# Optimization experiments

Hardware: AMD Instinct MI355X
Metric: run time of the kernel (lower is better)

Reference implementation:

```python
import jax, jax.numpy as jnp
import numpy as np

B, S, D, H, E, K = 2, 1024, 512, 2048, 64, 2
EPS = 1e-5


def setup_inputs() -> dict:
    key = jax.random.key(0)
    ks = jax.random.split(key, 5)
    s = 0.02  # small init scale for stability
    return {
        "x": jax.random.normal(ks[0], (B, S, D), dtype=jnp.float32),
        "Wg": jax.random.normal(ks[1], (D, E), dtype=jnp.float32) * s,
        "bg": jnp.zeros((E,), dtype=jnp.float32),
        "W1": jax.random.normal(ks[2], (E, D, H), dtype=jnp.float32) * s,
        "b1": jnp.zeros((E, H), dtype=jnp.float32),
        "W2": jax.random.normal(ks[3], (E, H, D), dtype=jnp.float32) * s,
        "b2": jnp.zeros((E, D), dtype=jnp.float32),
        "gamma": jnp.ones((D,), dtype=jnp.float32),
        "beta": jnp.zeros((D,), dtype=jnp.float32),
    }


def reference(x, Wg, bg, W1, b1, W2, b2, gamma, beta):
    # Gating: softmax over experts, keep top-k weights, zero the rest (scatter)
    probs = jax.nn.softmax(x @ Wg + bg, axis=-1)          # [B,S,E]
    topk_vals, topk_idx = jax.lax.top_k(probs, K)          # [B,S,K]
    sparse_w = jnp.sum(
        jax.nn.one_hot(topk_idx, E, dtype=probs.dtype) * topk_vals[..., None],
        axis=-2,
    )                                                      # [B,S,E]

    # Dense MoE: run every expert FFN on every token (faithful to source)
    h = jax.nn.relu(jnp.einsum('bsd,edh->bseh', x, W1) + b1)   # [B,S,E,H]
    expert_out = jnp.einsum('bseh,ehd->bsed', h, W2) + b2      # [B,S,E,D]

    # Weighted combine + residual
    out = jnp.einsum('bse,bsed->bsd', sparse_w, expert_out) + x

    # LayerNorm (eps=1e-5, elementwise affine)
    mu = out.mean(-1, keepdims=True)
    var = ((out - mu) ** 2).mean(-1, keepdims=True)
    return (out - mu) * jax.lax.rsqrt(var + EPS) * gamma + beta
```

## Files before the change

kernel.cpp:

```cpp
#include <hip/hip_runtime.h>
#include <hip/hip_bf16.h>

#define NTOK 2048
#define DIM 512
#define HID 2048
#define NEXP 64
#define NSLICE 8
#define HSLICE 256
#define TT 64
#define LN_EPS 1e-5f

#define WS_OFF 0
#define HS_OFF 20480
#define SMEM_BYTES 53248

typedef __bf16 bf16x8 __attribute__((ext_vector_type(8)));
typedef float f32x4 __attribute__((ext_vector_type(4)));

__global__ void init_kernel(float4* __restrict__ accb, int* __restrict__ counts) {
    int i = blockIdx.x * blockDim.x + threadIdx.x;
    accb[i] = make_float4(0.f, 0.f, 0.f, 0.f);
    if (i < NEXP) counts[i] = 0;
}

__global__ void gate_kernel(const float* __restrict__ x,
                            const float* __restrict__ Wg,
                            const float* __restrict__ bg,
                            int* __restrict__ counts,
                            int* __restrict__ btok,
                            float* __restrict__ bw) {
    const int t = blockIdx.x;
    const int lane = threadIdx.x;
    __shared__ float xs[DIM];
    const float4* xrow = (const float4*)(x + (size_t)t * DIM);
    ((float4*)xs)[lane] = xrow[lane];
    ((float4*)xs)[lane + 64] = xrow[lane + 64];
    __syncthreads();

    float acc = bg[lane];
    #pragma unroll 8
    for (int d = 0; d < DIM; d++) acc += xs[d] * Wg[d * NEXP + lane];

    float m = acc;
    #pragma unroll
    for (int off = 32; off; off >>= 1) m = fmaxf(m, __shfl_xor(m, off));
    float p = __expf(acc - m);
    float ssum = p;
    #pragma unroll
    for (int off = 32; off; off >>= 1) ssum += __shfl_xor(ssum, off);
    float prob = p / ssum;

    float v1 = prob; int i1 = lane;
    #pragma unroll
    for (int off = 32; off; off >>= 1) {
        float ov = __shfl_xor(v1, off);
        int   oi = __shfl_xor(i1, off);
        if (ov > v1 || (ov == v1 && oi < i1)) { v1 = ov; i1 = oi; }
    }
    float v2 = (lane == i1) ? -1e30f : prob; int i2 = lane;
    #pragma unroll
    for (int off = 32; off; off >>= 1) {
        float ov = __shfl_xor(v2, off);
        int   oi = __shfl_xor(i2, off);
        if (ov > v2 || (ov == v2 && oi < i2)) { v2 = ov; i2 = oi; }
    }

    if (lane == 0) {
        int s0 = atomicAdd(&counts[i1], 1);
        btok[i1 * NTOK + s0] = t;  bw[i1 * NTOK + s0] = v1;
        int s1 = atomicAdd(&counts[i2], 1);
        btok[i2 * NTOK + s1] = t;  bw[i2 * NTOK + s1] = v2;
    }
}

__device__ __forceinline__ void stage_w(const float* __restrict__ src, size_t rs,
                                        __bf16* __restrict__ wsb, int tid) {
    #pragma unroll
    for (int kh = 0; kh < 2; kh++) {
        float v[16];
        #pragma unroll
        for (int u = 0; u < 16; u++)
            v[u] = src[(size_t)(kh * 16 + u) * rs + tid];
        #pragma unroll
        for (int kg = 0; kg < 2; kg++) {
            bf16x8 pk;
            #pragma unroll
            for (int j = 0; j < 8; j++) pk[j] = (__bf16)v[kg * 8 + j];
            *(bf16x8*)(wsb + tid * 40 + (kh * 2 + kg) * 8) = pk;
        }
    }
}

__global__ __launch_bounds__(256, 3) void ffn_kernel(
    const float* __restrict__ x,
    const float* __restrict__ W1, const float* __restrict__ b1,
    const float* __restrict__ W2, const float* __restrict__ b2,
    const int* __restrict__ counts,
    const int* __restrict__ btok, const float* __restrict__ bw,
    float* __restrict__ accb)
{
    __shared__ char smem[SMEM_BYTES];
    __bf16* wsb = (__bf16*)(smem + WS_OFF);

    const int e = blockIdx.x >> 3;
    const int s = blockIdx.x & 7;
    const int n = counts[e];
    if (n <= 0) return;

    const int tid  = threadIdx.x;
    const int lane = tid & 63;
    const int wid  = tid >> 6;
    const int lq   = lane >> 4;
    const int lm   = lane & 15;

    const float* W1e = W1 + (size_t)e * DIM * HID;
    const float* W2e = W2 + (size_t)e * HID * DIM;
    const int*   btoke = btok + e * NTOK;
    const float* bwe   = bw   + e * NTOK;

    for (int t0 = 0; t0 < n; t0 += TT) {
        const int tiln = min(TT, n - t0);

        int  toks[4];
        bool tv[4];
        #pragma unroll
        for (int mt = 0; mt < 4; mt++) {
            int tr = mt * 16 + lm;
            tv[mt] = tr < tiln;
            toks[mt] = tv[mt] ? btoke[t0 + tr] : 0;
        }

        f32x4 acc[4][4];
        #pragma unroll
        for (int i = 0; i < 4; i++)
            #pragma unroll
            for (int j = 0; j < 4; j++) acc[i][j] = (f32x4)0.0f;

        for (int ks = 0; ks < 16; ks++) {
            __syncthreads();
            stage_w(W1e + (size_t)(ks * 32) * HID + s * HSLICE, HID, wsb, tid);
            __syncthreads();

            bf16x8 af[4];
            #pragma unroll
            for (int mt = 0; mt < 4; mt++) {
                if (tv[mt]) {
                    const float* xp = x + (size_t)toks[mt] * DIM + ks * 32 + lq * 8;
                    float4 f0 = *(const float4*)(xp);
                    float4 f1 = *(const float4*)(xp + 4);
                    bf16x8 v;
                    v[0]=(__bf16)f0.x; v[1]=(__bf16)f0.y; v[2]=(__bf16)f0.z; v[3]=(__bf16)f0.w;
                    v[4]=(__bf16)f1.x; v[5]=(__bf16)f1.y; v[6]=(__bf16)f1.z; v[7]=(__bf16)f1.w;
                    af[mt] = v;
                } else {
                    af[mt] = (bf16x8)0.0f;
                }
            }
            #pragma unroll
            for (int nt = 0; nt < 4; nt++) {
                bf16x8 bfv = *(const bf16x8*)(wsb + (wid * 64 + nt * 16 + lm) * 40 + lq * 8);
                #pragma unroll
                for (int mt = 0; mt < 4; mt++)
                    acc[nt][mt] = __builtin_amdgcn_mfma_f32_16x16x32_bf16(
                        af[mt], bfv, acc[nt][mt], 0, 0, 0);
            }
        }

        __syncthreads();
        #pragma unroll
        for (int nt = 0; nt < 4; nt++) {
            int hloc0 = wid * 64 + nt * 16 + lm;
            float b1v = b1[e * HID + s * HSLICE + hloc0];
            #pragma unroll
            for (int mt = 0; mt < 4; mt++) {
                #pragma unroll
                for (int r = 0; r < 4; r++) {
                    int tr = mt * 16 + lq * 4 + r;
                    float v = fmaxf(acc[nt][mt][r] + b1v, 0.f);
                    *(__bf16*)(smem + HS_OFF + tr * 512 +
                               (((hloc0 >> 3) ^ (tr & 7)) * 16) + (hloc0 & 7) * 2) = (__bf16)v;
                }
            }
        }

        for (int dh = 0; dh < 2; dh++) {
            f32x4 yacc[4][4];
            #pragma unroll
            for (int i = 0; i < 4; i++)
                #pragma unroll
                for (int j = 0; j < 4; j++) yacc[i][j] = (f32x4)0.0f;

            for (int ks = 0; ks < 8; ks++) {
                __syncthreads();
                stage_w(W2e + (size_t)(s * HSLICE + ks * 32) * DIM + dh * 256, DIM, wsb, tid);
                __syncthreads();

                bf16x8 af[4];
                int kcA = ks * 4 + lq;
                #pragma unroll
                for (int mt = 0; mt < 4; mt++) {
                    int tr = mt * 16 + lm;
                    af[mt] = *(const bf16x8*)(smem + HS_OFF + tr * 512 + ((kcA ^ (tr & 7)) * 16));
                }
                #pragma unroll
                for (int nt = 0; nt < 4; nt++) {
                    bf16x8 bfv = *(const bf16x8*)(wsb + (wid * 64 + nt * 16 + lm) * 40 + lq * 8);
                    #pragma unroll
                    for (int mt = 0; mt < 4; mt++)
                        yacc[nt][mt] = __builtin_amdgcn_mfma_f32_16x16x32_bf16(
                            af[mt], bfv, yacc[nt][mt], 0, 0, 0);
                }
            }
            float b2s[4];
            #pragma unroll
            for (int nt = 0; nt < 4; nt++) {
                int d = dh * 256 + wid * 64 + nt * 16 + lm;
                b2s[nt] = (s == 0) ? b2[e * DIM + d] : 0.f;
            }
            #pragma unroll
            for (int mt = 0; mt < 4; mt++) {
                #pragma unroll
                for (int r = 0; r < 4; r++) {
                    int tr = mt * 16 + lq * 4 + r;
                    if (tr < tiln) {
                        int tok = btoke[t0 + tr];
                        float w = bwe[t0 + tr];
                        float* dst = accb + (size_t)tok * DIM;
                        #pragma unroll
                        for (int nt = 0; nt < 4; nt++) {
                            int d = dh * 256 + wid * 64 + nt * 16 + lm;
                            atomicAdd(dst + d, w * (yacc[nt][mt][r] + b2s[nt]));
                        }
                    }
                }
            }
        }
        __syncthreads();
    }
}

__global__ void ln_kernel(const float* __restrict__ x,
                          const float* __restrict__ accb,
                          const float* __restrict__ gamma,
                          const float* __restrict__ beta,
                          float* __restrict__ out) {
    const int t = blockIdx.x;
    const int tid = threadIdx.x;
    __shared__ float red[8];
    const size_t base = (size_t)t * DIM;
    float v0 = x[base + tid] + accb[base + tid];
    float v1 = x[base + 256 + tid] + accb[base + 256 + tid];
    float s  = v0 + v1;
    float sq = v0 * v0 + v1 * v1;
    #pragma unroll
    for (int off = 32; off; off >>= 1) { s += __shfl_xor(s, off); sq += __shfl_xor(sq, off); }
    if ((tid & 63) == 0) { red[tid >> 6] = s; red[4 + (tid >> 6)] = sq; }
    __syncthreads();
    float S  = red[0] + red[1] + red[2] + red[3];
    float SQ = red[4] + red[5] + red[6] + red[7];
    float mu  = S * (1.f / DIM);
    float var = SQ * (1.f / DIM) - mu * mu;
    float inv = rsqrtf(var + LN_EPS);
    out[base + tid]       = (v0 - mu) * inv * gamma[tid]       + beta[tid];
    out[base + 256 + tid] = (v1 - mu) * inv * gamma[256 + tid] + beta[256 + tid];
}

extern "C" void kernel_launch(void* const* d_in, const int* in_sizes, int n_in,
                              void* d_out, int out_size, void* d_ws, size_t ws_size,
                              hipStream_t stream) {
    const float* x     = (const float*)d_in[0];
    const float* Wg    = (const float*)d_in[1];
    const float* bg    = (const float*)d_in[2];
    const float* W1    = (const float*)d_in[3];
    const float* b1    = (const float*)d_in[4];
    const float* W2    = (const float*)d_in[5];
    const float* b2    = (const float*)d_in[6];
    const float* gamma = (const float*)d_in[7];
    const float* beta  = (const float*)d_in[8];

    char* ws = (char*)d_ws;
    int*   counts = (int*)ws;
    int*   btok   = (int*)(ws + 4096);
    float* bwv    = (float*)(ws + 4096 + 524288);
    float* accb   = (float*)(ws + 4096 + 2 * 524288);

    init_kernel<<<1024, 256, 0, stream>>>((float4*)accb, counts);
    gate_kernel<<<NTOK, 64, 0, stream>>>(x, Wg, bg, counts, btok, bwv);
    ffn_kernel<<<NEXP * NSLICE, 256, 0, stream>>>(x, W1, b1, W2, b2,
                                                  counts, btok, bwv, accb);
    ln_kernel<<<NTOK, 256, 0, stream>>>(x, accb, gamma, beta, (float*)d_out);
}
```

Baseline: 745.7 us.

## Double-buffer weight staging with register prefetch and single-barrier MFMA loops

Weight tiles for both FFN GEMMs move to two LDS buffers. The next tile is loaded into registers as float4 and written to the idle buffer while MFMAs run on the current one, so each step needs one lgkmcnt barrier instead of two syncthreads. Activation loads from x are also prefetched one k-step ahead, and the W2 loop is flattened into 16 steps so the pipeline spans both D halves. The weight LDS layout gets an XOR swizzle with coalesced float4 global reads. The cost is more LDS and registers, with launch bounds lowered from 3 to 2 blocks per CU, which reduces occupancy.

```diff
diff --git a/kernel.cpp b/kernel.cpp
--- a/kernel.cpp
+++ b/kernel.cpp
@@ -10,12 +10,19 @@
 #define TT 64
 #define LN_EPS 1e-5f
 
-#define WS_OFF 0
-#define HS_OFF 20480
-#define SMEM_BYTES 53248
+#define WS0_OFF 0
+#define WS1_OFF 20480
+#define HS_OFF  40960
+#define SMEM_BYTES 73728
 
 typedef __bf16 bf16x8 __attribute__((ext_vector_type(8)));
 typedef float f32x4 __attribute__((ext_vector_type(4)));
+
+#define LGKM_BARRIER() do { \
+    asm volatile("s_waitcnt lgkmcnt(0)" ::: "memory"); \
+    __builtin_amdgcn_s_barrier(); \
+    asm volatile("" ::: "memory"); \
+} while (0)
 
 __global__ void init_kernel(float4* __restrict__ accb, int* __restrict__ counts) {
     int i = blockIdx.x * blockDim.x + threadIdx.x;
@@ -73,25 +80,55 @@
     }
 }
 
-__device__ __forceinline__ void stage_w(const float* __restrict__ src, size_t rs,
-                                        __bf16* __restrict__ wsb, int tid) {
-    #pragma unroll
-    for (int kh = 0; kh < 2; kh++) {
-        float v[16];
-        #pragma unroll
-        for (int u = 0; u < 16; u++)
-            v[u] = src[(size_t)(kh * 16 + u) * rs + tid];
-        #pragma unroll
-        for (int kg = 0; kg < 2; kg++) {
-            bf16x8 pk;
-            #pragma unroll
-            for (int j = 0; j < 8; j++) pk[j] = (__bf16)v[kg * 8 + j];
-            *(bf16x8*)(wsb + tid * 40 + (kh * 2 + kg) * 8) = pk;
-        }
-    }
-}
-
-__global__ __launch_bounds__(256, 3) void ffn_kernel(
+__device__ __forceinline__ int ws_off(int col, int kg) {
+    return col * 40 + ((kg ^ ((col >> 3) & 3)) << 3);
+}
+
+__device__ __forceinline__ void wload(const float* __restrict__ src, size_t rs,
+                                      int wid, int lane, float4 v[8]) {
+    const float* p = src + (size_t)(wid * 8) * rs + lane * 4;
+    #pragma unroll
+    for (int u = 0; u < 8; u++) v[u] = *(const float4*)(p + (size_t)u * rs);
+}
+
+__device__ __forceinline__ void wstore(__bf16* __restrict__ wsb,
+                                       int wid, int lane, const float4 v[8]) {
+    #pragma unroll
+    for (int j = 0; j < 4; j++) {
+        bf16x8 pk;
+        #pragma unroll
+        for (int u = 0; u < 8; u++) {
+            const float* f = (const float*)&v[u];
+            pk[u] = (__bf16)f[j];
+        }
+        *(bf16x8*)(wsb + ws_off(lane * 4 + j, wid)) = pk;
+    }
+}
+
+__device__ __forceinline__ void aload(const float* __restrict__ x,
+                                      const int toks[4], int ks, int lq,
+                                      float4 ar[4][2]) {
+    #pragma unroll
+    for (int mt = 0; mt < 4; mt++) {
+        const float* xp = x + (size_t)toks[mt] * DIM + ks * 32 + lq * 8;
+        ar[mt][0] = *(const float4*)xp;
+        ar[mt][1] = *(const float4*)(xp + 4);
+    }
+}
+
+__device__ __forceinline__ void acvt(const float4 ar[4][2], bf16x8 af[4]) {
+    #pragma unroll
+    for (int mt = 0; mt < 4; mt++) {
+        bf16x8 v;
+        const float* f0 = (const float*)&ar[mt][0];
+        const float* f1 = (const float*)&ar[mt][1];
+        #pragma unroll
+        for (int j = 0; j < 4; j++) { v[j] = (__bf16)f0[j]; v[4 + j] = (__bf16)f1[j]; }
+        af[mt] = v;
+    }
+}
+
+__global__ __launch_bounds__(256, 2) void ffn_kernel(
     const float* __restrict__ x,
     const float* __restrict__ W1, const float* __restrict__ b1,
     const float* __restrict__ W2, const float* __restrict__ b2,
@@ -100,7 +137,8 @@
     float* __restrict__ accb)
 {
     __shared__ char smem[SMEM_BYTES];
-    __bf16* wsb = (__bf16*)(smem + WS_OFF);
+    __bf16* ws0 = (__bf16*)(smem + WS0_OFF);
+    __bf16* ws1 = (__bf16*)(smem + WS1_OFF);
 
     const int e = blockIdx.x >> 3;
     const int s = blockIdx.x & 7;
@@ -113,21 +151,19 @@
     const int lq   = lane >> 4;
     const int lm   = lane & 15;
 
-    const float* W1e = W1 + (size_t)e * DIM * HID;
-    const float* W2e = W2 + (size_t)e * HID * DIM;
+    const float* W1s = W1 + (size_t)e * DIM * HID + s * HSLICE;
+    const float* W2s = W2 + ((size_t)e * HID + (size_t)s * HSLICE) * DIM;
     const int*   btoke = btok + e * NTOK;
     const float* bwe   = bw   + e * NTOK;
 
     for (int t0 = 0; t0 < n; t0 += TT) {
         const int tiln = min(TT, n - t0);
 
-        int  toks[4];
-        bool tv[4];
+        int toks[4];
         #pragma unroll
         for (int mt = 0; mt < 4; mt++) {
             int tr = mt * 16 + lm;
-            tv[mt] = tr < tiln;
-            toks[mt] = tv[mt] ? btoke[t0 + tr] : 0;
+            toks[mt] = (tr < tiln) ? btoke[t0 + tr] : btoke[t0];
         }
 
         f32x4 acc[4][4];
@@ -136,37 +172,40 @@
             #pragma unroll
             for (int j = 0; j < 4; j++) acc[i][j] = (f32x4)0.0f;
 
+        float4 wv[8];
+        float4 ar[4][2];
+
+        wload(W1s, HID, wid, lane, wv);
+        aload(x, toks, 0, lq, ar);
+        wstore(ws0, wid, lane, wv);
+        wload(W1s + (size_t)32 * HID, HID, wid, lane, wv);
+        LGKM_BARRIER();
+        int cur = 0;
+
         for (int ks = 0; ks < 16; ks++) {
-            __syncthreads();
-            stage_w(W1e + (size_t)(ks * 32) * HID + s * HSLICE, HID, wsb, tid);
-            __syncthreads();
-
             bf16x8 af[4];
-            #pragma unroll
-            for (int mt = 0; mt < 4; mt++) {
-                if (tv[mt]) {
-                    const float* xp = x + (size_t)toks[mt] * DIM + ks * 32 + lq * 8;
-                    float4 f0 = *(const float4*)(xp);
-                    float4 f1 = *(const float4*)(xp + 4);
-                    bf16x8 v;
-                    v[0]=(__bf16)f0.x; v[1]=(__bf16)f0.y; v[2]=(__bf16)f0.z; v[3]=(__bf16)f0.w;
-                    v[4]=(__bf16)f1.x; v[5]=(__bf16)f1.y; v[6]=(__bf16)f1.z; v[7]=(__bf16)f1.w;
-                    af[mt] = v;
-                } else {
-                    af[mt] = (bf16x8)0.0f;
-                }
-            }
+            acvt(ar, af);
+            if (ks < 15) aload(x, toks, ks + 1, lq, ar);
+
+            const __bf16* wr = cur ? ws1 : ws0;
             #pragma unroll
             for (int nt = 0; nt < 4; nt++) {
-                bf16x8 bfv = *(const bf16x8*)(wsb + (wid * 64 + nt * 16 + lm) * 40 + lq * 8);
+                bf16x8 bfv = *(const bf16x8*)(wr + ws_off(wid * 64 + nt * 16 + lm, lq));
                 #pragma unroll
                 for (int mt = 0; mt < 4; mt++)
                     acc[nt][mt] = __builtin_amdgcn_mfma_f32_16x16x32_bf16(
                         af[mt], bfv, acc[nt][mt], 0, 0, 0);
             }
-        }
-
-        __syncthreads();
+            if (ks < 15) {
+                __bf16* ww = cur ? ws0 : ws1;
+                wstore(ww, wid, lane, wv);
+                if (ks < 14)
+                    wload(W1s + (size_t)((ks + 2) * 32) * HID, HID, wid, lane, wv);
+                LGKM_BARRIER();
+                cur ^= 1;
+            }
+        }
+
         #pragma unroll
         for (int nt = 0; nt < 4; nt++) {
             int hloc0 = wid * 64 + nt * 16 + lm;
@@ -183,59 +222,75 @@
             }
         }
 
-        for (int dh = 0; dh < 2; dh++) {
-            f32x4 yacc[4][4];
-            #pragma unroll
-            for (int i = 0; i < 4; i++)
-                #pragma unroll
-                for (int j = 0; j < 4; j++) yacc[i][j] = (f32x4)0.0f;
-
-            for (int ks = 0; ks < 8; ks++) {
-                __syncthreads();
-                stage_w(W2e + (size_t)(s * HSLICE + ks * 32) * DIM + dh * 256, DIM, wsb, tid);
-                __syncthreads();
-
-                bf16x8 af[4];
-                int kcA = ks * 4 + lq;
+        f32x4 yacc[4][4];
+        wload(W2s, DIM, wid, lane, wv);
+        wstore(ws0, wid, lane, wv);
+        wload(W2s + (size_t)32 * DIM, DIM, wid, lane, wv);
+        LGKM_BARRIER();
+        cur = 0;
+
+        for (int u = 0; u < 16; u++) {
+            const int kk = u & 7, dh = u >> 3;
+            if (kk == 0) {
+                #pragma unroll
+                for (int i = 0; i < 4; i++)
+                    #pragma unroll
+                    for (int j = 0; j < 4; j++) yacc[i][j] = (f32x4)0.0f;
+            }
+
+            bf16x8 af[4];
+            const int kcA = kk * 4 + lq;
+            #pragma unroll
+            for (int mt = 0; mt < 4; mt++) {
+                int tr = mt * 16 + lm;
+                af[mt] = *(const bf16x8*)(smem + HS_OFF + tr * 512 + ((kcA ^ (tr & 7)) * 16));
+            }
+            const __bf16* wr = cur ? ws1 : ws0;
+            #pragma unroll
+            for (int nt = 0; nt < 4; nt++) {
+                bf16x8 bfv = *(const bf16x8*)(wr + ws_off(wid * 64 + nt * 16 + lm, lq));
+                #pragma unroll
+                for (int mt = 0; mt < 4; mt++)
+                    yacc[nt][mt] = __builtin_amdgcn_mfma_f32_16x16x32_bf16(
+                        af[mt], bfv, yacc[nt][mt], 0, 0, 0);
+            }
+            if (u < 15) {
+                __bf16* ww = cur ? ws0 : ws1;
+                wstore(ww, wid, lane, wv);
+                if (u < 14) {
+                    const int un = u + 2;
+                    wload(W2s + (size_t)((un & 7) * 32) * DIM + (un >> 3) * 256,
+                          DIM, wid, lane, wv);
+                }
+                LGKM_BARRIER();
+                cur ^= 1;
+            }
+            if (kk == 7) {
+                float b2s[4];
+                #pragma unroll
+                for (int nt = 0; nt < 4; nt++) {
+                    int d = dh * 256 + wid * 64 + nt * 16 + lm;
+                    b2s[nt] = (s == 0) ? b2[e * DIM + d] : 0.f;
+                }
                 #pragma unroll
                 for (int mt = 0; mt < 4; mt++) {
-                    int tr = mt * 16 + lm;
-                    af[mt] = *(const bf16x8*)(smem + HS_OFF + tr * 512 + ((kcA ^ (tr & 7)) * 16));
-                }
-                #pragma unroll
-                for (int nt = 0; nt < 4; nt++) {
-                    bf16x8 bfv = *(const bf16x8*)(wsb + (wid * 64 + nt * 16 + lm) * 40 + lq * 8);
                     #pragma unroll
-                    for (int mt = 0; mt < 4; mt++)
-                        yacc[nt][mt] = __builtin_amdgcn_mfma_f32_16x16x32_bf16(
-                            af[mt], bfv, yacc[nt][mt], 0, 0, 0);
-                }
-            }
-            float b2s[4];
-            #pragma unroll
-            for (int nt = 0; nt < 4; nt++) {
-                int d = dh * 256 + wid * 64 + nt * 16 + lm;
-                b2s[nt] = (s == 0) ? b2[e * DIM + d] : 0.f;
-            }
-            #pragma unroll
-            for (int mt = 0; mt < 4; mt++) {
-                #pragma unroll
-                for (int r = 0; r < 4; r++) {
-                    int tr = mt * 16 + lq * 4 + r;
-                    if (tr < tiln) {
-                        int tok = btoke[t0 + tr];
-                        float w = bwe[t0 + tr];
-                        float* dst = accb + (size_t)tok * DIM;
-                        #pragma unroll
-                        for (int nt = 0; nt < 4; nt++) {
-                            int d = dh * 256 + wid * 64 + nt * 16 + lm;
-                            atomicAdd(dst + d, w * (yacc[nt][mt][r] + b2s[nt]));
+                    for (int r = 0; r < 4; r++) {
+                        int tr = mt * 16 + lq * 4 + r;
+                        if (tr < tiln) {
+                            int tok = btoke[t0 + tr];
+                            float w = bwe[t0 + tr];
+                            float* dst = accb + (size_t)tok * DIM;
+                            #pragma unroll
+                            for (int nt = 0; nt < 4; nt++) {
+                                int d = dh * 256 + wid * 64 + nt * 16 + lm;
+                                atomicAdd(dst + d, w * (yacc[nt][mt][r] + b2s[nt]));
+                            }
                         }
                     }
                 }
             }
         }
-        __syncthreads();
     }
 }
 
```

Result: no change. 756.3 us (+1.4%).

## Split hidden dim into 16 slices and rework weight staging per wave

Applied to the files above, without the earlier changes.

Doubles the number of hidden-dimension slices per expert (16×128 instead of 8×256) so twice as many blocks run, and halves shared memory to allow higher occupancy (launch bounds 4). Each wave now owns 16 token rows across all 128 hidden columns rather than 64 rows × 64 columns. Weight staging uses float4 global loads prefetched into registers before the barrier, plus an XOR-swizzled shared layout to reduce bank conflicts. In exchange, each weight tile is reused across fewer tokens per wave, the second GEMM runs in four output quarters with more barriers, and partial-sum atomics into the output buffer double.

```diff
diff --git a/kernel.cpp b/kernel.cpp
--- a/kernel.cpp
+++ b/kernel.cpp
@@ -5,16 +5,17 @@
 #define DIM 512
 #define HID 2048
 #define NEXP 64
-#define NSLICE 8
-#define HSLICE 256
+#define NSLICE 16
+#define HSLICE 128
 #define TT 64
 #define LN_EPS 1e-5f
 
 #define WS_OFF 0
-#define HS_OFF 20480
-#define SMEM_BYTES 53248
+#define HS_OFF 10240
+#define SMEM_BYTES 26624
 
 typedef __bf16 bf16x8 __attribute__((ext_vector_type(8)));
+typedef __bf16 bf16x4 __attribute__((ext_vector_type(4)));
 typedef float f32x4 __attribute__((ext_vector_type(4)));
 
 __global__ void init_kernel(float4* __restrict__ accb, int* __restrict__ counts) {
@@ -73,25 +74,11 @@
     }
 }
 
-__device__ __forceinline__ void stage_w(const float* __restrict__ src, size_t rs,
-                                        __bf16* __restrict__ wsb, int tid) {
-    #pragma unroll
-    for (int kh = 0; kh < 2; kh++) {
-        float v[16];
-        #pragma unroll
-        for (int u = 0; u < 16; u++)
-            v[u] = src[(size_t)(kh * 16 + u) * rs + tid];
-        #pragma unroll
-        for (int kg = 0; kg < 2; kg++) {
-            bf16x8 pk;
-            #pragma unroll
-            for (int j = 0; j < 8; j++) pk[j] = (__bf16)v[kg * 8 + j];
-            *(bf16x8*)(wsb + tid * 40 + (kh * 2 + kg) * 8) = pk;
-        }
-    }
-}
-
-__global__ __launch_bounds__(256, 3) void ffn_kernel(
+__device__ __forceinline__ int ws_off(int col, int kg) {
+    return col * 40 + ((kg ^ ((col >> 3) & 3)) << 3);
+}
+
+__global__ __launch_bounds__(256, 4) void ffn_kernel(
     const float* __restrict__ x,
     const float* __restrict__ W1, const float* __restrict__ b1,
     const float* __restrict__ W2, const float* __restrict__ b2,
@@ -102,8 +89,8 @@
     __shared__ char smem[SMEM_BYTES];
     __bf16* wsb = (__bf16*)(smem + WS_OFF);
 
-    const int e = blockIdx.x >> 3;
-    const int s = blockIdx.x & 7;
+    const int e = blockIdx.x >> 4;
+    const int s = blockIdx.x & 15;
     const int n = counts[e];
     if (n <= 0) return;
 
@@ -112,125 +99,127 @@
     const int wid  = tid >> 6;
     const int lq   = lane >> 4;
     const int lm   = lane & 15;
-
-    const float* W1e = W1 + (size_t)e * DIM * HID;
-    const float* W2e = W2 + (size_t)e * HID * DIM;
+    const int c0   = (tid & 31) * 4;
+    const int r0   = (tid >> 5) * 4;
+
+    const float* W1s = W1 + (size_t)e * DIM * HID + s * HSLICE;
+    const float* W2s = W2 + ((size_t)e * HID + (size_t)s * HSLICE) * DIM;
     const int*   btoke = btok + e * NTOK;
     const float* bwe   = bw   + e * NTOK;
 
     for (int t0 = 0; t0 < n; t0 += TT) {
         const int tiln = min(TT, n - t0);
 
-        int  toks[4];
-        bool tv[4];
+        const int tra = wid * 16 + lm;
+        const int tok = btoke[t0 + (tra < tiln ? tra : 0)];
+        const float* xrow = x + (size_t)tok * DIM;
+
+        f32x4 acc[8];
         #pragma unroll
-        for (int mt = 0; mt < 4; mt++) {
-            int tr = mt * 16 + lm;
-            tv[mt] = tr < tiln;
-            toks[mt] = tv[mt] ? btoke[t0 + tr] : 0;
+        for (int i = 0; i < 8; i++) acc[i] = (f32x4)0.0f;
+
+        for (int ks = 0; ks < 16; ks++) {
+            float4 wv[4];
+            const float* wp = W1s + (size_t)(ks * 32 + r0) * HID + c0;
+            #pragma unroll
+            for (int u = 0; u < 4; u++) wv[u] = *(const float4*)(wp + (size_t)u * HID);
+            float4 a0 = *(const float4*)(xrow + ks * 32 + lq * 8);
+            float4 a1 = *(const float4*)(xrow + ks * 32 + lq * 8 + 4);
+
+            __syncthreads();
+            #pragma unroll
+            for (int j = 0; j < 4; j++) {
+                const float* f0 = (const float*)&wv[0];
+                const float* f1 = (const float*)&wv[1];
+                const float* f2 = (const float*)&wv[2];
+                const float* f3 = (const float*)&wv[3];
+                bf16x4 pk;
+                pk[0] = (__bf16)f0[j]; pk[1] = (__bf16)f1[j];
+                pk[2] = (__bf16)f2[j]; pk[3] = (__bf16)f3[j];
+                *(bf16x4*)(wsb + ws_off(c0 + j, r0 >> 3) + (r0 & 7)) = pk;
+            }
+            bf16x8 af;
+            {
+                const float* f0 = (const float*)&a0;
+                const float* f1 = (const float*)&a1;
+                #pragma unroll
+                for (int j = 0; j < 4; j++) { af[j] = (__bf16)f0[j]; af[4 + j] = (__bf16)f1[j]; }
+            }
+            __syncthreads();
+
+            #pragma unroll
+            for (int nt = 0; nt < 8; nt++) {
+                bf16x8 bfv = *(const bf16x8*)(wsb + ws_off(nt * 16 + lm, lq));
+                acc[nt] = __builtin_amdgcn_mfma_f32_16x16x32_bf16(af, bfv, acc[nt], 0, 0, 0);
+            }
         }
 
-        f32x4 acc[4][4];
         #pragma unroll
-        for (int i = 0; i < 4; i++)
-            #pragma unroll
-            for (int j = 0; j < 4; j++) acc[i][j] = (f32x4)0.0f;
-
-        for (int ks = 0; ks < 16; ks++) {
-            __syncthreads();
-            stage_w(W1e + (size_t)(ks * 32) * HID + s * HSLICE, HID, wsb, tid);
-            __syncthreads();
-
-            bf16x8 af[4];
-            #pragma unroll
-            for (int mt = 0; mt < 4; mt++) {
-                if (tv[mt]) {
-                    const float* xp = x + (size_t)toks[mt] * DIM + ks * 32 + lq * 8;
-                    float4 f0 = *(const float4*)(xp);
-                    float4 f1 = *(const float4*)(xp + 4);
-                    bf16x8 v;
-                    v[0]=(__bf16)f0.x; v[1]=(__bf16)f0.y; v[2]=(__bf16)f0.z; v[3]=(__bf16)f0.w;
-                    v[4]=(__bf16)f1.x; v[5]=(__bf16)f1.y; v[6]=(__bf16)f1.z; v[7]=(__bf16)f1.w;
-                    af[mt] = v;
-                } else {
-                    af[mt] = (bf16x8)0.0f;
+        for (int nt = 0; nt < 8; nt++) {
+            int hloc = nt * 16 + lm;
+            float b1v = b1[e * HID + s * HSLICE + hloc];
+            #pragma unroll
+            for (int r = 0; r < 4; r++) {
+                int tr = wid * 16 + lq * 4 + r;
+                float v = fmaxf(acc[nt][r] + b1v, 0.f);
+                *(__bf16*)(smem + HS_OFF + tr * 256 +
+                           (((hloc >> 3) ^ (tr & 7)) * 16) + (hloc & 7) * 2) = (__bf16)v;
+            }
+        }
+
+        for (int dq = 0; dq < 4; dq++) {
+            f32x4 yacc[8];
+            #pragma unroll
+            for (int i = 0; i < 8; i++) yacc[i] = (f32x4)0.0f;
+
+            for (int ks = 0; ks < 4; ks++) {
+                float4 wv[4];
+                const float* wp = W2s + (size_t)(ks * 32 + r0) * DIM + dq * 128 + c0;
+                #pragma unroll
+                for (int u = 0; u < 4; u++) wv[u] = *(const float4*)(wp + (size_t)u * DIM);
+
+                const int trb = wid * 16 + lm;
+                bf16x8 af = *(const bf16x8*)(smem + HS_OFF + trb * 256 +
+                                             (((ks * 4 + lq) ^ (trb & 7)) * 16));
+
+                __syncthreads();
+                #pragma unroll
+                for (int j = 0; j < 4; j++) {
+                    const float* f0 = (const float*)&wv[0];
+                    const float* f1 = (const float*)&wv[1];
+                    const float* f2 = (const float*)&wv[2];
+                    const float* f3 = (const float*)&wv[3];
+                    bf16x4 pk;
+                    pk[0] = (__bf16)f0[j]; pk[1] = (__bf16)f1[j];
+                    pk[2] = (__bf16)f2[j]; pk[3] = (__bf16)f3[j];
+                    *(bf16x4*)(wsb + ws_off(c0 + j, r0 >> 3) + (r0 & 7)) = pk;
                 }
-            }
-            #pragma unroll
-            for (int nt = 0; nt < 4; nt++) {
-                bf16x8 bfv = *(const bf16x8*)(wsb + (wid * 64 + nt * 16 + lm) * 40 + lq * 8);
-                #pragma unroll
-                for (int mt = 0; mt < 4; mt++)
-                    acc[nt][mt] = __builtin_amdgcn_mfma_f32_16x16x32_bf16(
-                        af[mt], bfv, acc[nt][mt], 0, 0, 0);
-            }
-        }
-
-        __syncthreads();
-        #pragma unroll
-        for (int nt = 0; nt < 4; nt++) {
-            int hloc0 = wid * 64 + nt * 16 + lm;
-            float b1v = b1[e * HID + s * HSLICE + hloc0];
-            #pragma unroll
-            for (int mt = 0; mt < 4; mt++) {
-                #pragma unroll
-                for (int r = 0; r < 4; r++) {
-                    int tr = mt * 16 + lq * 4 + r;
-                    float v = fmaxf(acc[nt][mt][r] + b1v, 0.f);
-                    *(__bf16*)(smem + HS_OFF + tr * 512 +
-                               (((hloc0 >> 3) ^ (tr & 7)) * 16) + (hloc0 & 7) * 2) = (__bf16)v;
+                __syncthreads();
+
+                #pragma unroll
+                for (int nt = 0; nt < 8; nt++) {
+                    bf16x8 bfv = *(const bf16x8*)(wsb + ws_off(nt * 16 + lm, lq));
+                    yacc[nt] = __builtin_amdgcn_mfma_f32_16x16x32_bf16(af, bfv, yacc[nt], 0, 0, 0);
                 }
             }
-        }
-
-        for (int dh = 0; dh < 2; dh++) {
-            f32x4 yacc[4][4];
-            #pragma unroll
-            for (int i = 0; i < 4; i++)
-                #pragma unroll
-                for (int j = 0; j < 4; j++) yacc[i][j] = (f32x4)0.0f;
-
-            for (int ks = 0; ks < 8; ks++) {
-                __syncthreads();
-                stage_w(W2e + (size_t)(s * HSLICE + ks * 32) * DIM + dh * 256, DIM, wsb, tid);
-                __syncthreads();
-
-                bf16x8 af[4];
-                int kcA = ks * 4 + lq;
-                #pragma unroll
-                for (int mt = 0; mt < 4; mt++) {
-                    int tr = mt * 16 + lm;
-                    af[mt] = *(const bf16x8*)(smem + HS_OFF + tr * 512 + ((kcA ^ (tr & 7)) * 16));
-                }
-                #pragma unroll
-                for (int nt = 0; nt < 4; nt++) {
-                    bf16x8 bfv = *(const bf16x8*)(wsb + (wid * 64 + nt * 16 + lm) * 40 + lq * 8);
+
+            float b2s[8];
+            #pragma unroll
+            for (int nt = 0; nt < 8; nt++) {
+                int d = dq * 128 + nt * 16 + lm;
+                b2s[nt] = (s == 0) ? b2[e * DIM + d] : 0.f;
+            }
+            #pragma unroll
+            for (int r = 0; r < 4; r++) {
+                int tr = wid * 16 + lq * 4 + r;
+                if (tr < tiln) {
+                    int tok2 = btoke[t0 + tr];
+                    float w = bwe[t0 + tr];
+                    float* dst = accb + (size_t)tok2 * DIM;
                     #pragma unroll
-                    for (int mt = 0; mt < 4; mt++)
-                        yacc[nt][mt] = __builtin_amdgcn_mfma_f32_16x16x32_bf16(
-                            af[mt], bfv, yacc[nt][mt], 0, 0, 0);
-                }
-            }
-            float b2s[4];
-            #pragma unroll
-            for (int nt = 0; nt < 4; nt++) {
-                int d = dh * 256 + wid * 64 + nt * 16 + lm;
-                b2s[nt] = (s == 0) ? b2[e * DIM + d] : 0.f;
-            }
-            #pragma unroll
-            for (int mt = 0; mt < 4; mt++) {
-                #pragma unroll
-                for (int r = 0; r < 4; r++) {
-                    int tr = mt * 16 + lq * 4 + r;
-                    if (tr < tiln) {
-                        int tok = btoke[t0 + tr];
-                        float w = bwe[t0 + tr];
-                        float* dst = accb + (size_t)tok * DIM;
-                        #pragma unroll
-                        for (int nt = 0; nt < 4; nt++) {
-                            int d = dh * 256 + wid * 64 + nt * 16 + lm;
-                            atomicAdd(dst + d, w * (yacc[nt][mt][r] + b2s[nt]));
-                        }
+                    for (int nt = 0; nt < 8; nt++) {
+                        int d = dq * 128 + nt * 16 + lm;
+                        atomicAdd(dst + d, w * (yacc[nt][r] + b2s[nt]));
                     }
                 }
             }
```

Result: faster. 684.0 us (-8.3%).
